# Kernel tuning notes

Hardware: AMD Instinct MI355X
Metric: run time of the kernel (lower is better)

Reference implementation:

```python
import jax, jax.numpy as jnp
import numpy as np
from jax import lax

LEAKY_ALPHA = 0.2  # tf.nn.leaky_relu default


def setup_inputs() -> dict:
    key = jax.random.key(0)
    k1, k2, k3 = jax.random.split(key, 3)
    B, C, D, H, W = 8, 2, 96, 64, 64
    F, d, h, w = 8, 3, 60, 64
    inputs = jax.random.normal(k1, (B, C, D, H, W), dtype=jnp.float32)
    # weight/bias correspond to tf variables [F,1,c,d,h,w] with the singleton squeezed
    weight = jax.random.normal(k2, (F, C, d, h, w), dtype=jnp.float32) * 0.05
    bias = jax.random.normal(k3, (F, C, d, h, w), dtype=jnp.float32) * 0.05
    return {"inputs": inputs, "weight": weight, "bias": bias}


def reference(inputs, weight, bias):
    B, C, D, H, W = inputs.shape
    F, _, d, h, w = weight.shape
    margin = H - h
    Dout = D - d + 1  # depth positions where tf.slice succeeds

    # sliding depth windows: xwin[b,c,i,k,:,:] = inputs[b,c,i+k,:,:] -> [B,C,Dout,d,H,W]
    xwin = jnp.stack([inputs[:, :, k:k + Dout] for k in range(d)], axis=3)
    # margin accumulation over H (sum of margin+1 shifted h-slices): [B,C,Dout,d,h,W]
    s = xwin[..., 0:h, :]
    for j in range(1, margin + 1):
        s = s + xwin[..., j:j + h, :]
    s = jnp.moveaxis(s, 2, 1)  # [B,Dout,C,d,h,w]

    # y = (sum_j x_slice_j * w + b) * 0.25 -> a[b,f,i,c,k,p,q]
    a = (s[:, None] * weight[None, :, None] + bias[None, :, None]) * 0.25
    # a: [B,F,Dout,C,d,h,w]

    # fixed ones-kernel conv3d, filters=1, SAME, strides (d,1,1), then leaky_relu
    a_r = a.reshape(B * F * Dout, C, d, h, w)
    kernel = jnp.ones((1, C, 3, 3, 3), dtype=a_r.dtype)
    conv = lax.conv_general_dilated(
        a_r, kernel, window_strides=(d, 1, 1), padding='SAME',
        dimension_numbers=('NCDHW', 'OIDHW', 'NCDHW'))  # [N,1,1,h,w]
    out = jax.nn.leaky_relu(conv, negative_slope=LEAKY_ALPHA)
    return out.reshape(B, F, Dout, h, w)
```

## Files before the change

kernel.cpp:

```cpp
#include <hip/hip_runtime.h>

#define B_ 8
#define C_ 2
#define D_ 96
#define H_ 64
#define W_ 64
#define F_ 8
#define KD 3
#define h_ 60
#define Dout_ 94
#define PLANE (h_ * W_)
#define NCH (PLANE / 4)
#define TD 4
#define NTILE ((Dout_ + TD - 1) / TD)
#define NS2 (B_ * C_ * D_)
#define S2_FLOATS ((size_t)NS2 * PLANE)

__device__ __forceinline__ float4 hsum3(float4 V, int col4) {
    const int lane = threadIdx.x & 63;
    float lw = __shfl(V.w, (lane + 63) & 63, 64);
    float rx = __shfl(V.x, (lane + 1) & 63, 64);
    if (col4 == 0) lw = 0.f;
    if (col4 == 15) rx = 0.f;
    float4 o;
    o.x = lw + V.x + V.y;
    o.y = V.x + V.y + V.z;
    o.z = V.y + V.z + V.w;
    o.w = V.z + V.w + rx;
    return o;
}

__global__ __launch_bounds__(256) void k_prep(const float* __restrict__ in,
                                              const float* __restrict__ bs,
                                              float* __restrict__ s2,
                                              float* __restrict__ bb) {
    const int bx = blockIdx.x;
    const int tid = threadIdx.x;
    __shared__ float4 lds[H_ * 16];

    if (bx < NS2) {
        const float4* ip4 = (const float4*)(in + (size_t)bx * (H_ * W_));
        float4* op4 = (float4*)(s2 + (size_t)bx * PLANE);
#pragma unroll
        for (int k = 0; k < 4; ++k) lds[tid + 256 * k] = ip4[tid + 256 * k];
        __syncthreads();
#pragma unroll
        for (int k = 0; k < 4; ++k) {
            const int e = tid + 256 * k;
            if (e < NCH) {
                const int row = e >> 4, col = e & 15;
                float4 s = lds[row * 16 + col];
#pragma unroll
                for (int j = 1; j < 5; ++j) {
                    const float4 v = lds[(row + j) * 16 + col];
                    s.x += v.x; s.y += v.y; s.z += v.z; s.w += v.w;
                }
                op4[e] = s;
            }
        }
    } else {
        const int f = bx - NS2;
        float4* R = lds;
        if (tid < 32) {
            const int r = (tid >> 4) ? 61 : 0;
            R[r * 16 + (tid & 15)] = make_float4(0, 0, 0, 0);
        }
        const float4* bp = (const float4*)(bs + (size_t)f * (C_ * KD * PLANE));
#pragma unroll
        for (int k = 0; k < 4; ++k) {
            const int e = tid + 256 * k;
            if (e < NCH) {
                float4 s = make_float4(0, 0, 0, 0);
#pragma unroll
                for (int s6 = 0; s6 < 6; ++s6) {
                    const float4 v = bp[s6 * NCH + e];
                    s.x += v.x; s.y += v.y; s.z += v.z; s.w += v.w;
                }
                R[((e >> 4) + 1) * 16 + (e & 15)] = s;
            }
        }
        __syncthreads();
        float4* ob = (float4*)(bb + (size_t)f * PLANE);
#pragma unroll
        for (int k = 0; k < 4; ++k) {
            const int e = tid + 256 * k;
            if (e < NCH) {
                const int row = e >> 4, c4 = e & 15;
                const float4 a = R[row * 16 + c4];
                const float4 m = R[(row + 1) * 16 + c4];
                const float4 d = R[(row + 2) * 16 + c4];
                float4 V;
                V.x = a.x + m.x + d.x; V.y = a.y + m.y + d.y;
                V.z = a.z + m.z + d.z; V.w = a.w + m.w + d.w;
                ob[e] = hsum3(V, c4);
            }
        }
    }
}

__global__ __launch_bounds__(256) void k_main(const float* __restrict__ s2,
                                              const float* __restrict__ wt,
                                              const float* __restrict__ bb,
                                              float* __restrict__ out) {
    const int bx = blockIdx.x;
    const int tile = bx % NTILE;
    const int f = (bx / NTILE) % F_;
    const int b = bx / (NTILE * F_);
    const int d0 = tile * TD;
    const int tid = threadIdx.x;

    float4 wreg[6][4];
    const float4* wp = (const float4*)(wt + (size_t)f * (C_ * KD * PLANE));
#pragma unroll
    for (int s6 = 0; s6 < 6; ++s6)
#pragma unroll
        for (int k = 0; k < 4; ++k) {
            const int e = tid + 256 * k;
            wreg[s6][k] = (e < NCH) ? wp[s6 * NCH + e] : make_float4(0, 0, 0, 0);
        }

    __shared__ float4 R[2][62 * 16];
    if (tid < 32) {
        const int r = (tid >> 4) ? 61 : 0;
        R[0][r * 16 + (tid & 15)] = make_float4(0, 0, 0, 0);
        R[1][r * 16 + (tid & 15)] = make_float4(0, 0, 0, 0);
    }

    const float4* s2b = (const float4*)s2 + (size_t)(b * C_) * D_ * NCH;
    const float4* bbp = (const float4*)(bb + (size_t)f * PLANE);
    float* ob = out + (size_t)((b * F_ + f) * Dout_) * PLANE;

#pragma unroll
    for (int t = 0; t < TD; ++t) {
        const int dout = d0 + t;

        float4 acc[4];
#pragma unroll
        for (int k = 0; k < 4; ++k) acc[k] = make_float4(0, 0, 0, 0);

#pragma unroll
        for (int c = 0; c < C_; ++c)
#pragma unroll
            for (int z = 0; z < KD; ++z) {
                int p = dout + z; if (p > D_ - 1) p = D_ - 1;
                const float4* sp = s2b + (size_t)(c * D_ + p) * NCH;
#pragma unroll
                for (int k = 0; k < 4; ++k) {
                    const int e = tid + 256 * k;
                    if (e < NCH) {
                        const float4 v = sp[e];
                        const float4 w = wreg[c * KD + z][k];
                        acc[k].x += v.x * w.x; acc[k].y += v.y * w.y;
                        acc[k].z += v.z * w.z; acc[k].w += v.w * w.w;
                    }
                }
            }

        float4* Rb = R[t & 1];
#pragma unroll
        for (int k = 0; k < 4; ++k) {
            const int e = tid + 256 * k;
            if (e < NCH) Rb[((e >> 4) + 1) * 16 + (e & 15)] = acc[k];
        }
        __syncthreads();

        if (dout < Dout_) {
            float4* od4 = (float4*)(ob + (size_t)dout * PLANE);
#pragma unroll
            for (int k = 0; k < 4; ++k) {
                const int e = tid + 256 * k;
                if (e < NCH) {
                    const int row = e >> 4, c4 = e & 15;
                    const float4 a = Rb[row * 16 + c4];
                    const float4 m = Rb[(row + 1) * 16 + c4];
                    const float4 d = Rb[(row + 2) * 16 + c4];
                    float4 V;
                    V.x = a.x + m.x + d.x; V.y = a.y + m.y + d.y;
                    V.z = a.z + m.z + d.z; V.w = a.w + m.w + d.w;
                    float4 o = hsum3(V, c4);
                    const float4 bbv = bbp[e];
                    o.x = 0.25f * (o.x + bbv.x); o.y = 0.25f * (o.y + bbv.y);
                    o.z = 0.25f * (o.z + bbv.z); o.w = 0.25f * (o.w + bbv.w);
                    o.x = (o.x > 0.f) ? o.x : 0.2f * o.x;
                    o.y = (o.y > 0.f) ? o.y : 0.2f * o.y;
                    o.z = (o.z > 0.f) ? o.z : 0.2f * o.z;
                    o.w = (o.w > 0.f) ? o.w : 0.2f * o.w;
                    od4[e] = o;
                }
            }
        }
    }
}

extern "C" void kernel_launch(void* const* d_in, const int* in_sizes, int n_in,
                              void* d_out, int out_size, void* d_ws, size_t ws_size,
                              hipStream_t stream) {
    const float* in = (const float*)d_in[0];
    const float* wt = (const float*)d_in[1];
    const float* bs = (const float*)d_in[2];
    float* out = (float*)d_out;

    float* s2 = (float*)d_ws;
    float* bb = s2 + S2_FLOATS;

    k_prep<<<dim3(NS2 + F_), dim3(256), 0, stream>>>(in, bs, s2, bb);
    k_main<<<dim3(B_ * F_ * NTILE), dim3(256), 0, stream>>>(s2, wt, bb, out);
}
```

Baseline: 165.2 us.

## Retile main kernel into half-plane tiles with s2 reuse across filters

After: 208.2 us. +26.0%, slower.

```diff
diff --git a/kernel.cpp b/kernel.cpp
--- a/kernel.cpp
+++ b/kernel.cpp
@@ -11,17 +11,23 @@
 #define Dout_ 94
 #define PLANE (h_ * W_)
 #define NCH (PLANE / 4)
-#define TD 4
-#define NTILE ((Dout_ + TD - 1) / TD)
 #define NS2 (B_ * C_ * D_)
 #define S2_FLOATS ((size_t)NS2 * PLANE)
-
-__device__ __forceinline__ float4 hsum3(float4 V, int col4) {
+#define NDT (Dout_ / 2)
+#define FT 4
+#define NFG (F_ / FT)
+
+__device__ __forceinline__ float4 f4fma(float4 a, float4 b, float4 c) {
+    c.x += a.x * b.x; c.y += a.y * b.y; c.z += a.z * b.z; c.w += a.w * b.w;
+    return c;
+}
+
+__device__ __forceinline__ float4 hsum3(float4 V, int c4) {
     const int lane = threadIdx.x & 63;
     float lw = __shfl(V.w, (lane + 63) & 63, 64);
     float rx = __shfl(V.x, (lane + 1) & 63, 64);
-    if (col4 == 0) lw = 0.f;
-    if (col4 == 15) rx = 0.f;
+    if (c4 == 0) lw = 0.f;
+    if (c4 == 15) rx = 0.f;
     float4 o;
     o.x = lw + V.x + V.y;
     o.y = V.x + V.y + V.z;
@@ -103,89 +109,107 @@
                                               const float* __restrict__ bb,
                                               float* __restrict__ out) {
     const int bx = blockIdx.x;
-    const int tile = bx % NTILE;
-    const int f = (bx / NTILE) % F_;
-    const int b = bx / (NTILE * F_);
-    const int d0 = tile * TD;
+    const int fg = bx & 1;
+    const int yh = (bx >> 1) & 1;
+    const int dt = (bx >> 2) % NDT;
+    const int b  = bx / (4 * NDT);
+    const int dout0 = dt * 2;
+    const int f0 = fg * FT;
     const int tid = threadIdx.x;
 
-    float4 wreg[6][4];
-    const float4* wp = (const float4*)(wt + (size_t)f * (C_ * KD * PLANE));
-#pragma unroll
-    for (int s6 = 0; s6 < 6; ++s6)
-#pragma unroll
-        for (int k = 0; k < 4; ++k) {
-            const int e = tid + 256 * k;
-            wreg[s6][k] = (e < NCH) ? wp[s6 * NCH + e] : make_float4(0, 0, 0, 0);
-        }
-
-    __shared__ float4 R[2][62 * 16];
-    if (tid < 32) {
-        const int r = (tid >> 4) ? 61 : 0;
-        R[0][r * 16 + (tid & 15)] = make_float4(0, 0, 0, 0);
-        R[1][r * 16 + (tid & 15)] = make_float4(0, 0, 0, 0);
+    __shared__ float4 Rb[2][512];
+
+    int e[2], c4[2], gy[2], gyc[2];
+    bool valid[2], orow[2];
+#pragma unroll
+    for (int k = 0; k < 2; ++k) {
+        e[k] = tid + 256 * k;
+        const int r = e[k] >> 4;
+        c4[k] = e[k] & 15;
+        gy[k] = yh * 30 - 1 + r;
+        int g = gy[k]; g = (g < 0) ? 0 : g; g = (g > 59) ? 59 : g;
+        gyc[k] = g;
+        valid[k] = (gy[k] >= 0) && (gy[k] <= 59);
+        orow[k] = (r >= 1) && (r <= 30);
     }
 
-    const float4* s2b = (const float4*)s2 + (size_t)(b * C_) * D_ * NCH;
-    const float4* bbp = (const float4*)(bb + (size_t)f * PLANE);
-    float* ob = out + (size_t)((b * F_ + f) * Dout_) * PLANE;
-
-#pragma unroll
-    for (int t = 0; t < TD; ++t) {
-        const int dout = d0 + t;
-
-        float4 acc[4];
-#pragma unroll
-        for (int k = 0; k < 4; ++k) acc[k] = make_float4(0, 0, 0, 0);
-
-#pragma unroll
-        for (int c = 0; c < C_; ++c)
+    float4 s2r[2][4][2];
+    const float4* s2f = (const float4*)s2;
+#pragma unroll
+    for (int c = 0; c < 2; ++c)
+#pragma unroll
+        for (int zz = 0; zz < 4; ++zz) {
+            const size_t base = (size_t)((b * C_ + c) * D_ + dout0 + zz) * NCH;
+#pragma unroll
+            for (int k = 0; k < 2; ++k)
+                s2r[c][zz][k] = s2f[base + gyc[k] * 16 + c4[k]];
+        }
+
+    const float4* wtf = (const float4*)wt;
+    const float4* bbf = (const float4*)bb;
+    const float4 z4 = make_float4(0, 0, 0, 0);
+
+    for (int fi = 0; fi < FT; ++fi) {
+        const int f = f0 + fi;
+
+        float4 acc[2][2];
+#pragma unroll
+        for (int t = 0; t < 2; ++t)
+#pragma unroll
+            for (int k = 0; k < 2; ++k) acc[t][k] = z4;
+
+#pragma unroll
+        for (int c = 0; c < 2; ++c)
 #pragma unroll
             for (int z = 0; z < KD; ++z) {
-                int p = dout + z; if (p > D_ - 1) p = D_ - 1;
-                const float4* sp = s2b + (size_t)(c * D_ + p) * NCH;
-#pragma unroll
-                for (int k = 0; k < 4; ++k) {
-                    const int e = tid + 256 * k;
-                    if (e < NCH) {
-                        const float4 v = sp[e];
-                        const float4 w = wreg[c * KD + z][k];
-                        acc[k].x += v.x * w.x; acc[k].y += v.y * w.y;
-                        acc[k].z += v.z * w.z; acc[k].w += v.w * w.w;
-                    }
-                }
-            }
-
-        float4* Rb = R[t & 1];
-#pragma unroll
-        for (int k = 0; k < 4; ++k) {
-            const int e = tid + 256 * k;
-            if (e < NCH) Rb[((e >> 4) + 1) * 16 + (e & 15)] = acc[k];
-        }
-        __syncthreads();
-
-        if (dout < Dout_) {
-            float4* od4 = (float4*)(ob + (size_t)dout * PLANE);
-#pragma unroll
-            for (int k = 0; k < 4; ++k) {
-                const int e = tid + 256 * k;
-                if (e < NCH) {
-                    const int row = e >> 4, c4 = e & 15;
-                    const float4 a = Rb[row * 16 + c4];
-                    const float4 m = Rb[(row + 1) * 16 + c4];
-                    const float4 d = Rb[(row + 2) * 16 + c4];
-                    float4 V;
+                const size_t wbase = (size_t)((f * C_ + c) * KD + z) * NCH;
+                float4 w[2];
+#pragma unroll
+                for (int k = 0; k < 2; ++k)
+                    w[k] = wtf[wbase + gyc[k] * 16 + c4[k]];
+#pragma unroll
+                for (int k = 0; k < 2; ++k) {
+                    acc[0][k] = f4fma(w[k], s2r[c][z][k], acc[0][k]);
+                    acc[1][k] = f4fma(w[k], s2r[c][z + 1][k], acc[1][k]);
+                }
+            }
+
+        float4 bbv[2];
+#pragma unroll
+        for (int k = 0; k < 2; ++k)
+            bbv[k] = orow[k] ? bbf[(size_t)f * NCH + gy[k] * 16 + c4[k]] : z4;
+
+#pragma unroll
+        for (int t = 0; t < 2; ++t) {
+            float4* R = Rb[(fi * 2 + t) & 1];
+#pragma unroll
+            for (int k = 0; k < 2; ++k)
+                R[e[k]] = valid[k] ? acc[t][k] : z4;
+            __syncthreads();
+
+            const int dout = dout0 + t;
+            float4* of = (float4*)(out + (size_t)((b * F_ + f) * Dout_ + dout) * PLANE);
+#pragma unroll
+            for (int k = 0; k < 2; ++k) {
+                float4 V = z4;
+                if (orow[k]) {
+                    const float4 a = R[e[k] - 16];
+                    const float4 m = R[e[k]];
+                    const float4 d = R[e[k] + 16];
                     V.x = a.x + m.x + d.x; V.y = a.y + m.y + d.y;
                     V.z = a.z + m.z + d.z; V.w = a.w + m.w + d.w;
-                    float4 o = hsum3(V, c4);
-                    const float4 bbv = bbp[e];
-                    o.x = 0.25f * (o.x + bbv.x); o.y = 0.25f * (o.y + bbv.y);
-                    o.z = 0.25f * (o.z + bbv.z); o.w = 0.25f * (o.w + bbv.w);
+                }
+                float4 o = hsum3(V, c4[k]);
+                if (orow[k]) {
+                    o.x = 0.25f * (o.x + bbv[k].x);
+                    o.y = 0.25f * (o.y + bbv[k].y);
+                    o.z = 0.25f * (o.z + bbv[k].z);
+                    o.w = 0.25f * (o.w + bbv[k].w);
                     o.x = (o.x > 0.f) ? o.x : 0.2f * o.x;
                     o.y = (o.y > 0.f) ? o.y : 0.2f * o.y;
                     o.z = (o.z > 0.f) ? o.z : 0.2f * o.z;
                     o.w = (o.w > 0.f) ? o.w : 0.2f * o.w;
-                    od4[e] = o;
+                    of[gy[k] * 16 + c4[k]] = o;
                 }
             }
         }
@@ -204,5 +228,5 @@
     float* bb = s2 + S2_FLOATS;
 
     k_prep<<<dim3(NS2 + F_), dim3(256), 0, stream>>>(in, bs, s2, bb);
-    k_main<<<dim3(B_ * F_ * NTILE), dim3(256), 0, stream>>>(s2, wt, bb, out);
-}
+    k_main<<<dim3(B_ * NDT * 2 * NFG), dim3(256), 0, stream>>>(s2, wt, bb, out);
+}
```
